# Optimization experiments

Measured on AMD Instinct MI355X. Metric: run time of the kernel, lower is better.

The kernel has to match this reference:

```python
import jax, jax.numpy as jnp
import numpy as np

N_NODES = 100000
N_EDGES = 3200000
D_FEAT = 128
N1 = 128
N2 = 64
NUM_CLASSES = 10
NUM_GRAPHS = 256


def gcn_conv(x, edge_index, W, b, num_nodes):
    """PyG GCNConv: y = D^-1/2 (A+I) D^-1/2 (x W) + b, self-loops added."""
    src, dst = edge_index[0], edge_index[1]
    # degree including self-loop (edge weight 1)
    deg = jax.ops.segment_sum(jnp.ones_like(dst, dtype=x.dtype), dst,
                              num_segments=num_nodes) + 1.0
    dis = jnp.where(deg > 0, deg ** -0.5, 0.0)  # deg_inv_sqrt, [N]
    h = x @ W                                    # transform first, [N, out]
    norm = dis[src] * dis[dst]                   # [E]
    msg = h[src] * norm[:, None]                 # gather + scale, [E, out]
    agg = jax.ops.segment_sum(msg, dst, num_segments=num_nodes)
    agg = agg + h * (dis * dis)[:, None]         # self-loop contribution
    return agg + b


def global_mean_pool(x, batch, num_graphs):
    sums = jax.ops.segment_sum(x, batch, num_segments=num_graphs)
    cnt = jax.ops.segment_sum(jnp.ones((x.shape[0],), dtype=x.dtype), batch,
                              num_segments=num_graphs)
    return sums / jnp.maximum(cnt, 1.0)[:, None]


def setup_inputs() -> dict:
    key = jax.random.key(0)
    ks = jax.random.split(key, 8)
    x = jax.random.normal(ks[0], (N_NODES, D_FEAT), dtype=jnp.float32)
    edge_index = jax.random.randint(ks[1], (2, N_EDGES), 0, N_NODES, dtype=jnp.int64)
    batch = jnp.sort(jax.random.randint(ks[2], (N_NODES,), 0, NUM_GRAPHS, dtype=jnp.int64))
    W1 = jax.random.normal(ks[3], (D_FEAT, N1), dtype=jnp.float32) / np.sqrt(D_FEAT)
    b1 = jnp.zeros((N1,), dtype=jnp.float32)
    W2 = jax.random.normal(ks[4], (N1, N2), dtype=jnp.float32) / np.sqrt(N1)
    b2 = jnp.zeros((N2,), dtype=jnp.float32)
    Wfc = jax.random.normal(ks[5], (N2, NUM_CLASSES), dtype=jnp.float32) / np.sqrt(N2)
    bfc = jnp.zeros((NUM_CLASSES,), dtype=jnp.float32)
    return {"x": x, "edge_index": edge_index, "batch": batch,
            "W1": W1, "b1": b1, "W2": W2, "b2": b2,
            "Wfc": Wfc, "bfc": bfc, "num_graphs": NUM_GRAPHS}


def reference(x, edge_index, batch, W1, b1, W2, b2, Wfc, bfc, num_graphs):
    n = x.shape[0]
    h = gcn_conv(x, edge_index, W1, b1, n)
    h = jax.nn.relu(h)
    h = gcn_conv(h, edge_index, W2, b2, n)
    g = global_mean_pool(h, batch, num_graphs)   # [num_graphs, N2]
    # dropout is identity at inference
    return g @ Wfc + bfc                          # [num_graphs, num_classes]
```

## Files before the change

### kernel.cpp

```cpp
#include <hip/hip_runtime.h>
#include <math.h>

typedef unsigned int  u32;
typedef unsigned short u16;

#define TILE1 8192
#define BKW   256
#define CAP   9216

typedef __attribute__((ext_vector_type(8))) short bf16x8;
typedef __attribute__((ext_vector_type(4))) float f32x4;
typedef __attribute__((ext_vector_type(2))) float f32x2;
union frag_u { bf16x8 v; u32 u[4]; uint4 q; };

__device__ inline u32 bf16_rne(float f) {
    u32 u = __float_as_uint(f);
    return (u + 0x7FFFu + ((u >> 16) & 1u)) >> 16;
}
__device__ inline float bf_lo(u32 u) { return __uint_as_float(u << 16); }
__device__ inline float bf_hi(u32 u) { return __uint_as_float(u & 0xFFFF0000u); }

__device__ inline f32x2 up2(u32 u) {
    f32x2 t;
    t.x = __uint_as_float(u << 16);
    t.y = __uint_as_float(u & 0xFFFF0000u);
    return t;
}
__device__ inline void add8p(f32x2* a, uint4 q) {
    a[0] += up2(q.x); a[1] += up2(q.y); a[2] += up2(q.z); a[3] += up2(q.w);
}

__device__ inline u32 relu_pk(u32 v) {
    u32 s = v & 0x80008000u;
    u32 m = (s >> 15) * 0xFFFFu;
    return v & ~m;
}


__global__ __launch_bounds__(512) void k_part1(const int* __restrict__ ei,
                                               int* __restrict__ bucketCur,
                                               u32* __restrict__ tmp,
                                               int E, int N, int NBK) {
    __shared__ int hist[1024];
    __shared__ int base[512];
    const int tid = threadIdx.x;
    if (tid < NBK) { hist[tid] = 0; hist[512 + tid] = 0; }
    __syncthreads();

    const int rep = (tid & 1) << 9;
    const int t0 = blockIdx.x * TILE1;
    const int4* ei4s = (const int4*)ei;
    const int4* ei4d = (const int4*)(ei + E);
    const int q0 = t0 >> 2;
    const int QE = E >> 2;

    int sv[16], dv[16], key[16];
#pragma unroll
    for (int j = 0; j < 4; ++j) {
        int qi = q0 + j * 512 + tid;
        int4 s4 = make_int4(0, 0, 0, 0), d4 = make_int4(-1, -1, -1, -1);
        if (qi < QE) { s4 = ei4s[qi]; d4 = ei4d[qi]; }
        sv[4 * j + 0] = s4.x; dv[4 * j + 0] = d4.x;
        sv[4 * j + 1] = s4.y; dv[4 * j + 1] = d4.y;
        sv[4 * j + 2] = s4.z; dv[4 * j + 2] = d4.z;
        sv[4 * j + 3] = s4.w; dv[4 * j + 3] = d4.w;
    }
#pragma unroll
    for (int j = 0; j < 16; ++j) {
        key[j] = -1;
        if ((unsigned)dv[j] < (unsigned)N && (unsigned)sv[j] < (unsigned)N) {
            key[j] = dv[j] >> 8;
            atomicAdd(&hist[key[j] + rep], 1);
        }
    }
    __syncthreads();
    if (tid < NBK) {
        int tot = hist[tid] + hist[512 + tid];
        base[tid] = atomicAdd(&bucketCur[tid], tot);
        hist[tid] = 0;
    }
    __syncthreads();
#pragma unroll
    for (int j = 0; j < 16; ++j) {
        if (key[j] >= 0) {
            int slot = atomicAdd(&hist[key[j]], 1);
            int off = base[key[j]] + slot;
            if (off < CAP)
                tmp[(size_t)key[j] * CAP + off] =
                    ((u32)(dv[j] & 255) << 17) | (u32)sv[j];
        }
    }
}

__global__ __launch_bounds__(512) void k_part2(const int* __restrict__ bucketCnt,
                                               const u32* __restrict__ tmp,
                                               int* __restrict__ csr,
                                               int* __restrict__ rowptr,
                                               float* __restrict__ dis,
                                               int N, int NBK) {
    __shared__ int hist[256];
    __shared__ int ts[512];
    __shared__ int sStart;
    const int b = blockIdx.x;
    const int t = threadIdx.x;

    int myCnt = (t < NBK) ? bucketCnt[t] : 0;
    ts[t] = myCnt;
    __syncthreads();
    for (int off = 1; off < 512; off <<= 1) {
        int u = (t >= off) ? ts[t - off] : 0;
        __syncthreads();
        ts[t] += u;
        __syncthreads();
    }
    if (t == b) sStart = ts[t] - myCnt;
    if (b == 0 && t == NBK - 1) rowptr[N] = ts[t];
    __syncthreads();
    const int start = sStart;
    const int cnt = bucketCnt[b];
    const u32* src = tmp + (size_t)b * CAP;

    if (t < 256) hist[t] = 0;
    __syncthreads();
    for (int i = t; i < cnt; i += 512)
        atomicAdd(&hist[src[i] >> 17], 1);
    __syncthreads();

    int h = (t < 256) ? hist[t] : 0;
    ts[t] = h;
    __syncthreads();
    for (int off = 1; off < 512; off <<= 1) {
        int u = (t >= off) ? ts[t - off] : 0;
        __syncthreads();
        ts[t] += u;
        __syncthreads();
    }
    if (t < 256) hist[t] = ts[t] - h;
    __syncthreads();

    if (t < 256) {
        int gn = (b << 8) + t;
        if (gn < N) {
            int e0 = hist[t];
            int e1 = (t < 255) ? hist[t + 1] : cnt;
            rowptr[gn] = start + e0;
            dis[gn] = rsqrtf((float)(e1 - e0) + 1.0f);
        }
    }
    __syncthreads();

    for (int i = t; i < cnt; i += 512) {
        u32 v = src[i];
        int p = atomicAdd(&hist[v >> 17], 1);
        csr[start + p] = (int)(v & 0x1FFFFu);
    }
}


__global__ __launch_bounds__(256) void k_convW(
    const float* __restrict__ W1, const float* __restrict__ W2,
    u32* __restrict__ W1h, u32* __restrict__ W1l,
    u32* __restrict__ W2h, u32* __restrict__ W2l,
    int* __restrict__ bucketCur, int NBK)
{
    int idx = blockIdx.x * 256 + threadIdx.x;
    if (idx < NBK) bucketCur[idx] = 0;
    if (idx < 8192) {
        int n = idx >> 6, k = (idx & 63) * 2;
        float w0 = W1[k * 128 + n], w1 = W1[(k + 1) * 128 + n];
        u32 h0 = bf16_rne(w0), h1 = bf16_rne(w1);
        u32 l0 = bf16_rne(w0 - __uint_as_float(h0 << 16));
        u32 l1 = bf16_rne(w1 - __uint_as_float(h1 << 16));
        W1h[idx] = h0 | (h1 << 16);
        W1l[idx] = l0 | (l1 << 16);
    } else if (idx < 12288) {
        int i2 = idx - 8192;
        int n = i2 >> 6, k = (i2 & 63) * 2;
        float w0 = W2[k * 64 + n], w1 = W2[(k + 1) * 64 + n];
        u32 h0 = bf16_rne(w0), h1 = bf16_rne(w1);
        u32 l0 = bf16_rne(w0 - __uint_as_float(h0 << 16));
        u32 l1 = bf16_rne(w1 - __uint_as_float(h1 << 16));
        W2h[i2] = h0 | (h1 << 16);
        W2l[i2] = l0 | (l1 << 16);
    }
}


__global__ __launch_bounds__(256) void k_gemm1m(
    const float* __restrict__ X, const u32* __restrict__ Wh,
    const u32* __restrict__ Wl, const float* __restrict__ dis,
    u32* __restrict__ Hb, int M)
{
    __shared__ uint4 sW[4096];
    const int tid = threadIdx.x;
    const uint4* Wh4 = (const uint4*)Wh;
    const uint4* Wl4 = (const uint4*)Wl;
#pragma unroll
    for (int i = 0; i < 8; ++i) {
        int idx = tid + i * 256;
        int l = idx >> 4, j = idx & 15;
        int js = j ^ (l & 7);
        sW[l * 16 + js] = Wh4[idx];
        sW[2048 + l * 16 + js] = Wl4[idx];
    }
    __syncthreads();

    const int w = tid >> 6, lane = tid & 63;
    const int mrow = blockIdx.x * 64 + w * 16;
    const int m16 = lane & 15, quad = lane >> 4;
    int gm = mrow + m16; if (gm >= M) gm = M - 1;

    frag_u Ah[4], Al[4];
    const float* xr = X + (size_t)gm * 128;
#pragma unroll
    for (int kt = 0; kt < 4; ++kt) {
        int kb = kt * 32 + quad * 8;
        float4 xa = *(const float4*)(xr + kb);
        float4 xb = *(const float4*)(xr + kb + 4);
        float xe[8] = {xa.x, xa.y, xa.z, xa.w, xb.x, xb.y, xb.z, xb.w};
#pragma unroll
        for (int j = 0; j < 4; ++j) {
            u32 h0 = bf16_rne(xe[2 * j]),     h1 = bf16_rne(xe[2 * j + 1]);
            u32 l0 = bf16_rne(xe[2 * j]     - __uint_as_float(h0 << 16));
            u32 l1 = bf16_rne(xe[2 * j + 1] - __uint_as_float(h1 << 16));
            Ah[kt].u[j] = h0 | (h1 << 16);
            Al[kt].u[j] = l0 | (l1 << 16);
        }
    }

    float dv[4];
#pragma unroll
    for (int r = 0; r < 4; ++r) {
        int gR = mrow + quad * 4 + r;
        dv[r] = (gR < M) ? dis[gR] : 0.f;
    }

#pragma unroll
    for (int nt = 0; nt < 8; ++nt) {
        f32x4 acc = {0.f, 0.f, 0.f, 0.f};
        int l = nt * 16 + m16;
        int swz = l & 7;
#pragma unroll
        for (int kt = 0; kt < 4; ++kt) {
            frag_u Bh, Bl;
            int jb = (kt * 4 + quad) ^ swz;
            Bh.q = sW[l * 16 + jb];
            Bl.q = sW[2048 + l * 16 + jb];
            acc = __builtin_amdgcn_mfma_f32_16x16x32_bf16(Al[kt].v, Bh.v, acc, 0, 0, 0);
            acc = __builtin_amdgcn_mfma_f32_16x16x32_bf16(Ah[kt].v, Bl.v, acc, 0, 0, 0);
            acc = __builtin_amdgcn_mfma_f32_16x16x32_bf16(Ah[kt].v, Bh.v, acc, 0, 0, 0);
        }
#pragma unroll
        for (int r = 0; r < 4; ++r) {
            float vs = acc[r] * dv[r];
            float vo = __shfl_xor(vs, 1, 64);
            if ((m16 & 1) == 0) {
                int gR = mrow + quad * 4 + r;
                if (gR < M)
                    Hb[(size_t)gR * 64 + nt * 8 + (m16 >> 1)] =
                        bf16_rne(vs) | (bf16_rne(vo) << 16);
            }
        }
    }
}


__global__ __launch_bounds__(256) void k_gemm2m(
    const u32* __restrict__ Xb, const u32* __restrict__ Wh,
    const u32* __restrict__ Wl, const float* __restrict__ dis,
    u32* __restrict__ Hb, int M)
{
    __shared__ uint4 sW[2176];
    const int tid = threadIdx.x;
    const uint4* Wh4 = (const uint4*)Wh;
    const uint4* Wl4 = (const uint4*)Wl;
#pragma unroll
    for (int i = 0; i < 4; ++i) {
        int idx = tid + i * 256;
        int l = idx >> 4, j = idx & 15;
        sW[l * 17 + j] = Wh4[l * 16 + j];
        sW[1088 + l * 17 + j] = Wl4[l * 16 + j];
    }
    __syncthreads();

    const int w = tid >> 6, lane = tid & 63;
    const int mrow = blockIdx.x * 64 + w * 16;
    const int m16 = lane & 15, quad = lane >> 4;
    int gm = mrow + m16; if (gm >= M) gm = M - 1;

    const uint4* X4 = (const uint4*)Xb;
    frag_u A[4];
#pragma unroll
    for (int kt = 0; kt < 4; ++kt) {
        A[kt].q = X4[(size_t)gm * 16 + kt * 4 + quad];
#pragma unroll
        for (int j = 0; j < 4; ++j) A[kt].u[j] = relu_pk(A[kt].u[j]);
    }

    float dv[4];
#pragma unroll
    for (int r = 0; r < 4; ++r) {
        int gR = mrow + quad * 4 + r;
        dv[r] = (gR < M) ? dis[gR] : 0.f;
    }

#pragma unroll
    for (int nt = 0; nt < 4; ++nt) {
        f32x4 acc = {0.f, 0.f, 0.f, 0.f};
        int l = nt * 16 + m16;
#pragma unroll
        for (int kt = 0; kt < 4; ++kt) {
            frag_u Bh, Bl;
            Bh.q = sW[l * 17 + kt * 4 + quad];
            Bl.q = sW[1088 + l * 17 + kt * 4 + quad];
            acc = __builtin_amdgcn_mfma_f32_16x16x32_bf16(A[kt].v, Bl.v, acc, 0, 0, 0);
            acc = __builtin_amdgcn_mfma_f32_16x16x32_bf16(A[kt].v, Bh.v, acc, 0, 0, 0);
        }
#pragma unroll
        for (int r = 0; r < 4; ++r) {
            float vs = acc[r] * dv[r];
            float vo = __shfl_xor(vs, 1, 64);
            if ((m16 & 1) == 0) {
                int gR = mrow + quad * 4 + r;
                if (gR < M)
                    Hb[(size_t)gR * 32 + nt * 8 + (m16 >> 1)] =
                        bf16_rne(vs) | (bf16_rne(vo) << 16);
            }
        }
    }
}


template <int PART>
__global__ __launch_bounds__(256) void k_agg1h(
    const int* __restrict__ rowptr, const int* __restrict__ csr,
    const float* __restrict__ dis, const u32* __restrict__ Hb,
    const float* __restrict__ bias, u32* __restrict__ AGGb, int N)
{
    int n = (blockIdx.x * 256 + threadIdx.x) >> 6;
    int lane = threadIdx.x & 63;
    int slot = lane >> 3;
    int li   = lane & 7;
    if (n >= N) return;
    int e  = __builtin_amdgcn_readfirstlane(rowptr[n]);
    int s1 = __builtin_amdgcn_readfirstlane(rowptr[n + 1]);
    const float dn = dis[n];
    const char* hb = (const char*)Hb;
    const u32 offq = (u32)(PART * 128 + li * 16);

    f32x2 acc[4];
#pragma unroll
    for (int j = 0; j < 4; ++j) acc[j] = 0.f;

    for (; e + 32 <= s1; e += 32) {
        const int* c = csr + e;
        u32 b0 = (u32)c[slot]      << 8;
        u32 b1 = (u32)c[8 + slot]  << 8;
        u32 b2 = (u32)c[16 + slot] << 8;
        u32 b3 = (u32)c[24 + slot] << 8;
        uint4 q0 = *(const uint4*)(hb + b0 + offq);
        uint4 q1 = *(const uint4*)(hb + b1 + offq);
        uint4 q2 = *(const uint4*)(hb + b2 + offq);
        uint4 q3 = *(const uint4*)(hb + b3 + offq);
        add8p(acc, q0); add8p(acc, q1); add8p(acc, q2); add8p(acc, q3);
    }
    for (; e + 16 <= s1; e += 16) {
        const int* c = csr + e;
        u32 b0 = (u32)c[slot]     << 8;
        u32 b1 = (u32)c[8 + slot] << 8;
        uint4 q0 = *(const uint4*)(hb + b0 + offq);
        uint4 q1 = *(const uint4*)(hb + b1 + offq);
        add8p(acc, q0); add8p(acc, q1);
    }
    for (; e + 8 <= s1; e += 8) {
        u32 b0 = (u32)csr[e + slot] << 8;
        uint4 q0 = *(const uint4*)(hb + b0 + offq);
        add8p(acc, q0);
    }
    {
        int rem = s1 - e;
        int idx = -1;
        if (slot < rem) idx = csr[e + slot];
        else if (slot == rem) idx = n;
        if (idx >= 0) {
            uint4 qq = *(const uint4*)(hb + ((u32)idx << 8) + offq);
            add8p(acc, qq);
        }
    }

#pragma unroll
    for (int j = 0; j < 4; ++j) {
        acc[j].x += __shfl_xor(acc[j].x, 8, 64);
        acc[j].y += __shfl_xor(acc[j].y, 8, 64);
        acc[j].x += __shfl_xor(acc[j].x, 16, 64);
        acc[j].y += __shfl_xor(acc[j].y, 16, 64);
        acc[j].x += __shfl_xor(acc[j].x, 32, 64);
        acc[j].y += __shfl_xor(acc[j].y, 32, 64);
    }

    if (slot < 2) {
        const int q = PART * 8 + li;
        float4 bv = ((const float4*)bias)[q * 2 + slot];
        float o0 = fmaf(dn, acc[2 * slot + 0].x, bv.x);
        float o1 = fmaf(dn, acc[2 * slot + 0].y, bv.y);
        float o2 = fmaf(dn, acc[2 * slot + 1].x, bv.z);
        float o3 = fmaf(dn, acc[2 * slot + 1].y, bv.w);
        uint2 p;
        p.x = bf16_rne(o0) | (bf16_rne(o1) << 16);
        p.y = bf16_rne(o2) | (bf16_rne(o3) << 16);
        ((uint2*)AGGb)[(size_t)n * 32 + q * 2 + slot] = p;
    }
}


__global__ __launch_bounds__(256) void k_agg2(
    const int* __restrict__ rowptr, const int* __restrict__ csr,
    const float* __restrict__ dis, const u32* __restrict__ Hb,
    const float* __restrict__ bias, u32* __restrict__ AGGb, int N)
{
    int n = (blockIdx.x * 256 + threadIdx.x) >> 6;
    int lane = threadIdx.x & 63;
    int slot = lane >> 3;
    int li   = lane & 7;
    if (n >= N) return;
    int e  = __builtin_amdgcn_readfirstlane(rowptr[n]);
    int s1 = __builtin_amdgcn_readfirstlane(rowptr[n + 1]);
    const float dn = dis[n];
    const char* hb = (const char*)Hb;
    const u32 offq = (u32)li * 16u;

    f32x2 acc[4];
#pragma unroll
    for (int j = 0; j < 4; ++j) acc[j] = 0.f;

    for (; e + 32 <= s1; e += 32) {
        const int* c = csr + e;
        u32 b0 = (u32)c[slot]      << 7;
        u32 b1 = (u32)c[8 + slot]  << 7;
        u32 b2 = (u32)c[16 + slot] << 7;
        u32 b3 = (u32)c[24 + slot] << 7;
        uint4 q0 = *(const uint4*)(hb + b0 + offq);
        uint4 q1 = *(const uint4*)(hb + b1 + offq);
        uint4 q2 = *(const uint4*)(hb + b2 + offq);
        uint4 q3 = *(const uint4*)(hb + b3 + offq);
        add8p(acc, q0); add8p(acc, q1); add8p(acc, q2); add8p(acc, q3);
    }
    for (; e + 16 <= s1; e += 16) {
        const int* c = csr + e;
        u32 b0 = (u32)c[slot]     << 7;
        u32 b1 = (u32)c[8 + slot] << 7;
        uint4 q0 = *(const uint4*)(hb + b0 + offq);
        uint4 q1 = *(const uint4*)(hb + b1 + offq);
        add8p(acc, q0); add8p(acc, q1);
    }
    for (; e + 8 <= s1; e += 8) {
        u32 b0 = (u32)csr[e + slot] << 7;
        uint4 q0 = *(const uint4*)(hb + b0 + offq);
        add8p(acc, q0);
    }
    {
        int rem = s1 - e;
        int idx = -1;
        if (slot < rem) idx = csr[e + slot];
        else if (slot == rem) idx = n;
        if (idx >= 0) {
            uint4 qq = *(const uint4*)(hb + ((u32)idx << 7) + offq);
            add8p(acc, qq);
        }
    }

#pragma unroll
    for (int j = 0; j < 4; ++j) {
        acc[j].x += __shfl_xor(acc[j].x, 8, 64);
        acc[j].y += __shfl_xor(acc[j].y, 8, 64);
        acc[j].x += __shfl_xor(acc[j].x, 16, 64);
        acc[j].y += __shfl_xor(acc[j].y, 16, 64);
        acc[j].x += __shfl_xor(acc[j].x, 32, 64);
        acc[j].y += __shfl_xor(acc[j].y, 32, 64);
    }

    if (slot < 2) {
        float4 bv = ((const float4*)bias)[li * 2 + slot];
        float o0 = fmaf(dn, acc[2 * slot + 0].x, bv.x);
        float o1 = fmaf(dn, acc[2 * slot + 0].y, bv.y);
        float o2 = fmaf(dn, acc[2 * slot + 1].x, bv.z);
        float o3 = fmaf(dn, acc[2 * slot + 1].y, bv.w);
        uint2 p;
        p.x = bf16_rne(o0) | (bf16_rne(o1) << 16);
        p.y = bf16_rne(o2) | (bf16_rne(o3) << 16);
        ((uint2*)AGGb)[(size_t)n * 16 + li * 2 + slot] = p;
    }
}


__device__ inline int lower_bound(const int* __restrict__ b, int n, int v) {
    int lo = 0, hi = n;
    while (lo < hi) { int m = (lo + hi) >> 1; if (b[m] < v) lo = m + 1; else hi = m; }
    return lo;
}

__global__ __launch_bounds__(256) void k_poolfc(
    const int* __restrict__ batch, const u32* __restrict__ AGGb2,
    const float* __restrict__ Wfc, const float* __restrict__ bfc,
    float* __restrict__ out, int n)
{
    int g = blockIdx.x;
    int start = lower_bound(batch, n, g);
    int end   = lower_bound(batch, n, g + 1);
    int tid = threadIdx.x;
    int f = tid & 63, stripe = tid >> 6;
    int ui = f >> 1, hi = f & 1;
    float acc = 0.f;
    for (int i = start + stripe; i < end; i += 4) {
        u32 v = AGGb2[(size_t)i * 32 + ui];
        acc += hi ? bf_hi(v) : bf_lo(v);
    }
    __shared__ float red[256];
    __shared__ float mean[64];
    red[tid] = acc;
    __syncthreads();
    if (tid < 64) {
        float s = red[tid] + red[tid + 64] + red[tid + 128] + red[tid + 192];
        float c = (float)(end - start);
        mean[tid] = s / fmaxf(c, 1.0f);
    }
    __syncthreads();
    if (tid < 10) {
        float o = bfc[tid];
        for (int k = 0; k < 64; ++k)
            o = fmaf(mean[k], Wfc[k * 10 + tid], o);
        out[g * 10 + tid] = o;
    }
}


extern "C" void kernel_launch(void* const* d_in, const int* in_sizes, int n_in,
                              void* d_out, int out_size, void* d_ws, size_t ws_size,
                              hipStream_t stream)
{
    const float* x    = (const float*)d_in[0];
    const int*   ei   = (const int*)d_in[1];
    const int*   batch= (const int*)d_in[2];
    const float* W1   = (const float*)d_in[3];
    const float* b1   = (const float*)d_in[4];
    const float* W2   = (const float*)d_in[5];
    const float* b2   = (const float*)d_in[6];
    const float* Wfc  = (const float*)d_in[7];
    const float* bfc  = (const float*)d_in[8];
    float* out = (float*)d_out;

    const int N  = in_sizes[0] / 128;
    const int E  = in_sizes[1] / 2;
    const int ng = out_size / 10;

    const int NBK = (N + BKW - 1) / BKW;

    int*   rowptr    = (int*)d_ws;
    int*   bucketCur = rowptr + 102400;
    float* dis       = (float*)(bucketCur + 512);
    int*   csr       = (int*)(dis + 102400);
    u32*   tmp       = (u32*)(csr + E);
    u32*   Hb1       = tmp;
    u32*   agg2b     = tmp;
    u32*   agg1b     = (u32*)((int*)tmp + (size_t)N * 64);
    u16*   Hb2       = (u16*)((int*)agg1b + (size_t)N * 128);
    u32*   W1h       = (u32*)((int*)Hb2 + (size_t)N * 32);
    u32*   W1l       = W1h + 8192;
    u32*   W2h       = W1l + 8192;
    u32*   W2l       = W2h + 4096;

    k_convW<<<48, 256, 0, stream>>>(W1, W2, W1h, W1l, W2h, W2l, bucketCur, NBK);
    k_part1<<<(E + TILE1 - 1) / TILE1, 512, 0, stream>>>(ei, bucketCur, tmp, E, N, NBK);
    k_part2<<<NBK, 512, 0, stream>>>(bucketCur, tmp, csr, rowptr, dis, N, NBK);

    k_gemm1m<<<(N + 63) / 64, 256, 0, stream>>>(x, W1h, W1l, dis, Hb1, N);
    k_agg1h<0><<<(N + 3) / 4, 256, 0, stream>>>(rowptr, csr, dis, Hb1, b1, agg1b, N);
    k_agg1h<1><<<(N + 3) / 4, 256, 0, stream>>>(rowptr, csr, dis, Hb1, b1, agg1b, N);

    k_gemm2m<<<(N + 63) / 64, 256, 0, stream>>>(agg1b, W2h, W2l, dis, (u32*)Hb2, N);
    k_agg2<<<(N + 3) / 4, 256, 0, stream>>>(rowptr, csr, dis, (const u32*)Hb2, b2, agg2b, N);

    k_poolfc<<<ng, 256, 0, stream>>>(batch, agg2b, Wfc, bfc, out, N);
}
```

Baseline: 393.2 us.

## Sort nodes by degree and aggregate with small per-node thread groups

Adds a degree histogram in the CSR build, a prefix kernel and a scatter kernel that build a permutation of nodes grouped by in-degree. The two aggregation kernels are replaced by one templated kernel in which 16 or 8 threads handle a node's whole feature row, with each thread walking all of that node's edges. The old design used a 64-lane wave per node split into 8 edge slots, and layer 1 ran as two half-width passes. The new mapping is meant to balance work across waves and fetch each edge index once per node, at the cost of two extra small kernels and serial per-thread edge loops with uncoalesced index reads.

```diff
diff --git a/kernel.cpp b/kernel.cpp
--- a/kernel.cpp
+++ b/kernel.cpp
@@ -97,13 +97,16 @@
                                                int* __restrict__ csr,
                                                int* __restrict__ rowptr,
                                                float* __restrict__ dis,
+                                               int* __restrict__ gdegH,
                                                int N, int NBK) {
     __shared__ int hist[256];
     __shared__ int ts[512];
+    __shared__ int degh[256];
     __shared__ int sStart;
     const int b = blockIdx.x;
     const int t = threadIdx.x;
 
+    if (t < 256) degh[t] = 0;
     int myCnt = (t < NBK) ? bucketCnt[t] : 0;
     ts[t] = myCnt;
     __syncthreads();
@@ -144,10 +147,14 @@
             int e0 = hist[t];
             int e1 = (t < 255) ? hist[t + 1] : cnt;
             rowptr[gn] = start + e0;
-            dis[gn] = rsqrtf((float)(e1 - e0) + 1.0f);
-        }
-    }
-    __syncthreads();
+            int d = e1 - e0;
+            dis[gn] = rsqrtf((float)d + 1.0f);
+            atomicAdd(&degh[d < 255 ? d : 255], 1);
+        }
+    }
+    __syncthreads();
+
+    if (t < 256 && degh[t]) atomicAdd(&gdegH[t], degh[t]);
 
     for (int i = t; i < cnt; i += 512) {
         u32 v = src[i];
@@ -157,14 +164,53 @@
 }
 
 
+__global__ __launch_bounds__(256) void k_prefix(const int* __restrict__ gdegH,
+                                                int* __restrict__ binBase) {
+    __shared__ int ts[256];
+    int t = threadIdx.x;
+    int v = gdegH[t];
+    ts[t] = v;
+    __syncthreads();
+    for (int off = 1; off < 256; off <<= 1) {
+        int u = (t >= off) ? ts[t - off] : 0;
+        __syncthreads();
+        ts[t] += u;
+        __syncthreads();
+    }
+    binBase[t] = ts[t] - v;
+}
+
+__global__ __launch_bounds__(512) void k_scatter(const int* __restrict__ rowptr,
+                                                 int* __restrict__ binBase,
+                                                 int* __restrict__ perm, int N) {
+    __shared__ int lh[256];
+    __shared__ int lb[256];
+    int t = threadIdx.x;
+    int i = blockIdx.x * 512 + t;
+    if (t < 256) lh[t] = 0;
+    __syncthreads();
+    int d = 0, slot = 0;
+    if (i < N) {
+        d = rowptr[i + 1] - rowptr[i];
+        if (d > 255) d = 255;
+        slot = atomicAdd(&lh[d], 1);
+    }
+    __syncthreads();
+    if (t < 256) lb[t] = lh[t] ? atomicAdd(&binBase[t], lh[t]) : 0;
+    __syncthreads();
+    if (i < N) perm[lb[d] + slot] = i;
+}
+
+
 __global__ __launch_bounds__(256) void k_convW(
     const float* __restrict__ W1, const float* __restrict__ W2,
     u32* __restrict__ W1h, u32* __restrict__ W1l,
     u32* __restrict__ W2h, u32* __restrict__ W2l,
-    int* __restrict__ bucketCur, int NBK)
+    int* __restrict__ bucketCur, int* __restrict__ gdegH, int NBK)
 {
     int idx = blockIdx.x * 256 + threadIdx.x;
     if (idx < NBK) bucketCur[idx] = 0;
+    if (idx < 256) gdegH[idx] = 0;
     if (idx < 8192) {
         int n = idx >> 6, k = (idx & 63) * 2;
         float w0 = W1[k * 128 + n], w1 = W1[(k + 1) * 128 + n];
@@ -331,165 +377,75 @@
 }
 
 
-template <int PART>
-__global__ __launch_bounds__(256) void k_agg1h(
+template <int LGS>
+__global__ __launch_bounds__(256) void k_aggs(
     const int* __restrict__ rowptr, const int* __restrict__ csr,
-    const float* __restrict__ dis, const u32* __restrict__ Hb,
-    const float* __restrict__ bias, u32* __restrict__ AGGb, int N)
+    const int* __restrict__ perm, const float* __restrict__ dis,
+    const u32* __restrict__ Hb, const float* __restrict__ bias,
+    u32* __restrict__ AGGb, int N)
 {
-    int n = (blockIdx.x * 256 + threadIdx.x) >> 6;
-    int lane = threadIdx.x & 63;
-    int slot = lane >> 3;
-    int li   = lane & 7;
-    if (n >= N) return;
-    int e  = __builtin_amdgcn_readfirstlane(rowptr[n]);
-    int s1 = __builtin_amdgcn_readfirstlane(rowptr[n + 1]);
+    const int LG = 1 << LGS;
+    const int SH = LGS + 4;
+    int gid = blockIdx.x * 256 + threadIdx.x;
+    int s = gid >> LGS;
+    int li = threadIdx.x & (LG - 1);
+    if (s >= N) return;
+    int n = perm[s];
+    int e = rowptr[n];
+    int s1 = rowptr[n + 1];
     const float dn = dis[n];
     const char* hb = (const char*)Hb;
-    const u32 offq = (u32)(PART * 128 + li * 16);
+    const u32 off = (u32)li << 4;
 
     f32x2 acc[4];
 #pragma unroll
     for (int j = 0; j < 4; ++j) acc[j] = 0.f;
 
-    for (; e + 32 <= s1; e += 32) {
-        const int* c = csr + e;
-        u32 b0 = (u32)c[slot]      << 8;
-        u32 b1 = (u32)c[8 + slot]  << 8;
-        u32 b2 = (u32)c[16 + slot] << 8;
-        u32 b3 = (u32)c[24 + slot] << 8;
-        uint4 q0 = *(const uint4*)(hb + b0 + offq);
-        uint4 q1 = *(const uint4*)(hb + b1 + offq);
-        uint4 q2 = *(const uint4*)(hb + b2 + offq);
-        uint4 q3 = *(const uint4*)(hb + b3 + offq);
+    for (; e + 8 <= s1; e += 8) {
+        u32 b0 = (u32)csr[e + 0] << SH;
+        u32 b1 = (u32)csr[e + 1] << SH;
+        u32 b2 = (u32)csr[e + 2] << SH;
+        u32 b3 = (u32)csr[e + 3] << SH;
+        u32 b4 = (u32)csr[e + 4] << SH;
+        u32 b5 = (u32)csr[e + 5] << SH;
+        u32 b6 = (u32)csr[e + 6] << SH;
+        u32 b7 = (u32)csr[e + 7] << SH;
+        uint4 q0 = *(const uint4*)(hb + b0 + off);
+        uint4 q1 = *(const uint4*)(hb + b1 + off);
+        uint4 q2 = *(const uint4*)(hb + b2 + off);
+        uint4 q3 = *(const uint4*)(hb + b3 + off);
+        uint4 q4 = *(const uint4*)(hb + b4 + off);
+        uint4 q5 = *(const uint4*)(hb + b5 + off);
+        uint4 q6 = *(const uint4*)(hb + b6 + off);
+        uint4 q7 = *(const uint4*)(hb + b7 + off);
         add8p(acc, q0); add8p(acc, q1); add8p(acc, q2); add8p(acc, q3);
-    }
-    for (; e + 16 <= s1; e += 16) {
-        const int* c = csr + e;
-        u32 b0 = (u32)c[slot]     << 8;
-        u32 b1 = (u32)c[8 + slot] << 8;
-        uint4 q0 = *(const uint4*)(hb + b0 + offq);
-        uint4 q1 = *(const uint4*)(hb + b1 + offq);
+        add8p(acc, q4); add8p(acc, q5); add8p(acc, q6); add8p(acc, q7);
+    }
+    for (; e + 2 <= s1; e += 2) {
+        u32 b0 = (u32)csr[e + 0] << SH;
+        u32 b1 = (u32)csr[e + 1] << SH;
+        uint4 q0 = *(const uint4*)(hb + b0 + off);
+        uint4 q1 = *(const uint4*)(hb + b1 + off);
         add8p(acc, q0); add8p(acc, q1);
     }
-    for (; e + 8 <= s1; e += 8) {
-        u32 b0 = (u32)csr[e + slot] << 8;
-        uint4 q0 = *(const uint4*)(hb + b0 + offq);
+    if (e < s1) {
+        u32 b0 = (u32)csr[e] << SH;
+        uint4 q0 = *(const uint4*)(hb + b0 + off);
         add8p(acc, q0);
     }
     {
-        int rem = s1 - e;
-        int idx = -1;
-        if (slot < rem) idx = csr[e + slot];
-        else if (slot == rem) idx = n;
-        if (idx >= 0) {
-            uint4 qq = *(const uint4*)(hb + ((u32)idx << 8) + offq);
-            add8p(acc, qq);
-        }
-    }
-
-#pragma unroll
-    for (int j = 0; j < 4; ++j) {
-        acc[j].x += __shfl_xor(acc[j].x, 8, 64);
-        acc[j].y += __shfl_xor(acc[j].y, 8, 64);
-        acc[j].x += __shfl_xor(acc[j].x, 16, 64);
-        acc[j].y += __shfl_xor(acc[j].y, 16, 64);
-        acc[j].x += __shfl_xor(acc[j].x, 32, 64);
-        acc[j].y += __shfl_xor(acc[j].y, 32, 64);
-    }
-
-    if (slot < 2) {
-        const int q = PART * 8 + li;
-        float4 bv = ((const float4*)bias)[q * 2 + slot];
-        float o0 = fmaf(dn, acc[2 * slot + 0].x, bv.x);
-        float o1 = fmaf(dn, acc[2 * slot + 0].y, bv.y);
-        float o2 = fmaf(dn, acc[2 * slot + 1].x, bv.z);
-        float o3 = fmaf(dn, acc[2 * slot + 1].y, bv.w);
-        uint2 p;
-        p.x = bf16_rne(o0) | (bf16_rne(o1) << 16);
-        p.y = bf16_rne(o2) | (bf16_rne(o3) << 16);
-        ((uint2*)AGGb)[(size_t)n * 32 + q * 2 + slot] = p;
-    }
-}
-
-
-__global__ __launch_bounds__(256) void k_agg2(
-    const int* __restrict__ rowptr, const int* __restrict__ csr,
-    const float* __restrict__ dis, const u32* __restrict__ Hb,
-    const float* __restrict__ bias, u32* __restrict__ AGGb, int N)
-{
-    int n = (blockIdx.x * 256 + threadIdx.x) >> 6;
-    int lane = threadIdx.x & 63;
-    int slot = lane >> 3;
-    int li   = lane & 7;
-    if (n >= N) return;
-    int e  = __builtin_amdgcn_readfirstlane(rowptr[n]);
-    int s1 = __builtin_amdgcn_readfirstlane(rowptr[n + 1]);
-    const float dn = dis[n];
-    const char* hb = (const char*)Hb;
-    const u32 offq = (u32)li * 16u;
-
-    f32x2 acc[4];
-#pragma unroll
-    for (int j = 0; j < 4; ++j) acc[j] = 0.f;
-
-    for (; e + 32 <= s1; e += 32) {
-        const int* c = csr + e;
-        u32 b0 = (u32)c[slot]      << 7;
-        u32 b1 = (u32)c[8 + slot]  << 7;
-        u32 b2 = (u32)c[16 + slot] << 7;
-        u32 b3 = (u32)c[24 + slot] << 7;
-        uint4 q0 = *(const uint4*)(hb + b0 + offq);
-        uint4 q1 = *(const uint4*)(hb + b1 + offq);
-        uint4 q2 = *(const uint4*)(hb + b2 + offq);
-        uint4 q3 = *(const uint4*)(hb + b3 + offq);
-        add8p(acc, q0); add8p(acc, q1); add8p(acc, q2); add8p(acc, q3);
-    }
-    for (; e + 16 <= s1; e += 16) {
-        const int* c = csr + e;
-        u32 b0 = (u32)c[slot]     << 7;
-        u32 b1 = (u32)c[8 + slot] << 7;
-        uint4 q0 = *(const uint4*)(hb + b0 + offq);
-        uint4 q1 = *(const uint4*)(hb + b1 + offq);
-        add8p(acc, q0); add8p(acc, q1);
-    }
-    for (; e + 8 <= s1; e += 8) {
-        u32 b0 = (u32)csr[e + slot] << 7;
-        uint4 q0 = *(const uint4*)(hb + b0 + offq);
-        add8p(acc, q0);
-    }
-    {
-        int rem = s1 - e;
-        int idx = -1;
-        if (slot < rem) idx = csr[e + slot];
-        else if (slot == rem) idx = n;
-        if (idx >= 0) {
-            uint4 qq = *(const uint4*)(hb + ((u32)idx << 7) + offq);
-            add8p(acc, qq);
-        }
-    }
-
-#pragma unroll
-    for (int j = 0; j < 4; ++j) {
-        acc[j].x += __shfl_xor(acc[j].x, 8, 64);
-        acc[j].y += __shfl_xor(acc[j].y, 8, 64);
-        acc[j].x += __shfl_xor(acc[j].x, 16, 64);
-        acc[j].y += __shfl_xor(acc[j].y, 16, 64);
-        acc[j].x += __shfl_xor(acc[j].x, 32, 64);
-        acc[j].y += __shfl_xor(acc[j].y, 32, 64);
-    }
-
-    if (slot < 2) {
-        float4 bv = ((const float4*)bias)[li * 2 + slot];
-        float o0 = fmaf(dn, acc[2 * slot + 0].x, bv.x);
-        float o1 = fmaf(dn, acc[2 * slot + 0].y, bv.y);
-        float o2 = fmaf(dn, acc[2 * slot + 1].x, bv.z);
-        float o3 = fmaf(dn, acc[2 * slot + 1].y, bv.w);
-        uint2 p;
-        p.x = bf16_rne(o0) | (bf16_rne(o1) << 16);
-        p.y = bf16_rne(o2) | (bf16_rne(o3) << 16);
-        ((uint2*)AGGb)[(size_t)n * 16 + li * 2 + slot] = p;
-    }
+        uint4 q = *(const uint4*)(hb + ((u32)n << SH) + off);
+        add8p(acc, q);
+    }
+
+    float4 b0 = ((const float4*)bias)[li * 2 + 0];
+    float4 b1 = ((const float4*)bias)[li * 2 + 1];
+    uint4 p;
+    p.x = bf16_rne(fmaf(dn, acc[0].x, b0.x)) | (bf16_rne(fmaf(dn, acc[0].y, b0.y)) << 16);
+    p.y = bf16_rne(fmaf(dn, acc[1].x, b0.z)) | (bf16_rne(fmaf(dn, acc[1].y, b0.w)) << 16);
+    p.z = bf16_rne(fmaf(dn, acc[2].x, b1.x)) | (bf16_rne(fmaf(dn, acc[2].y, b1.y)) << 16);
+    p.w = bf16_rne(fmaf(dn, acc[3].x, b1.z)) | (bf16_rne(fmaf(dn, acc[3].y, b1.w)) << 16);
+    ((uint4*)AGGb)[(size_t)n * LG + li] = p;
 }
 
 
@@ -568,17 +524,21 @@
     u32*   W1l       = W1h + 8192;
     u32*   W2h       = W1l + 8192;
     u32*   W2l       = W2h + 4096;
-
-    k_convW<<<48, 256, 0, stream>>>(W1, W2, W1h, W1l, W2h, W2l, bucketCur, NBK);
+    int*   perm      = (int*)(W2l + 4096);
+    int*   gdegH     = perm + N;
+    int*   binBase   = gdegH + 256;
+
+    k_convW<<<48, 256, 0, stream>>>(W1, W2, W1h, W1l, W2h, W2l, bucketCur, gdegH, NBK);
     k_part1<<<(E + TILE1 - 1) / TILE1, 512, 0, stream>>>(ei, bucketCur, tmp, E, N, NBK);
-    k_part2<<<NBK, 512, 0, stream>>>(bucketCur, tmp, csr, rowptr, dis, N, NBK);
+    k_part2<<<NBK, 512, 0, stream>>>(bucketCur, tmp, csr, rowptr, dis, gdegH, N, NBK);
+    k_prefix<<<1, 256, 0, stream>>>(gdegH, binBase);
+    k_scatter<<<(N + 511) / 512, 512, 0, stream>>>(rowptr, binBase, perm, N);
 
     k_gemm1m<<<(N + 63) / 64, 256, 0, stream>>>(x, W1h, W1l, dis, Hb1, N);
-    k_agg1h<0><<<(N + 3) / 4, 256, 0, stream>>>(rowptr, csr, dis, Hb1, b1, agg1b, N);
-    k_agg1h<1><<<(N + 3) / 4, 256, 0, stream>>>(rowptr, csr, dis, Hb1, b1, agg1b, N);
+    k_aggs<4><<<(N * 16 + 255) / 256, 256, 0, stream>>>(rowptr, csr, perm, dis, Hb1, b1, agg1b, N);
 
     k_gemm2m<<<(N + 63) / 64, 256, 0, stream>>>(agg1b, W2h, W2l, dis, (u32*)Hb2, N);
-    k_agg2<<<(N + 3) / 4, 256, 0, stream>>>(rowptr, csr, dis, (const u32*)Hb2, b2, agg2b, N);
+    k_aggs<3><<<(N * 8 + 255) / 256, 256, 0, stream>>>(rowptr, csr, perm, dis, (const u32*)Hb2, b2, agg2b, N);
 
     k_poolfc<<<ng, 256, 0, stream>>>(batch, agg2b, Wfc, bfc, out, N);
 }
```

New measurement: 404.4 us. 1.03x slower.
